# Kernel optimization log

Measured on AMD Instinct MI355X. Metric: run time of the kernel, lower is better.

The kernel has to match this reference:

```python
import jax, jax.numpy as jnp
import numpy as np

PAD = 1          # kernel offsets lie in [-1, 1] for kernel_size=3
COORD_MAX = 128  # coordinates quantized to [0, 128)
S = COORD_MAX + 2 * PAD  # per-dimension encoding stride (130)


def setup_inputs() -> dict:
    key = jax.random.key(0)
    B, N, D = 4, 50000, 3
    coordinates = jax.random.randint(
        jax.random.fold_in(key, 0), (B, N, D), 0, COORD_MAX, dtype=jnp.int32)
    # batch_indices[b, n] == b, matching how the torch code partitions rows
    batch_indices = jnp.broadcast_to(jnp.arange(B, dtype=jnp.int32)[:, None], (B, N))
    # 3^3 hypercube kernel offsets, lexicographic order (KernelGenerator semantics)
    r = jnp.arange(-1, 2, dtype=jnp.int32)
    kernel_offsets = jnp.stack(jnp.meshgrid(r, r, r, indexing='ij'), axis=-1).reshape(-1, 3)
    return {"coordinates": coordinates, "batch_indices": batch_indices,
            "kernel_offsets": kernel_offsets}


def reference(coordinates, batch_indices, kernel_offsets):
    """Vectorized equivalent of LocalSelfAttention.compute_kernel_mapping.

    Returns (input_idx, output_idx, rel_pos_idx, output_key_tensor, num_unique).
    The first three are [B, N, K] (the torch kernel_map flattened row-major is
    exactly zip of these), output_key_tensor is [L, D] padded with -1 beyond
    num_unique rows, with unique keys in first-occurrence (insertion) order --
    identical to the Python dict-hashing loop.
    """
    B, N, D = coordinates.shape
    K = kernel_offsets.shape[0]
    L = B * N * K

    # neighbor coords per (point, offset): [B, N, K, D]
    nb = coordinates[:, :, None, :] + kernel_offsets[None, None, :, :]

    # encode (batch_id, neighbor_coord) into a single int32 key
    enc = jnp.broadcast_to(batch_indices[:, :, None], (B, N, K)).astype(jnp.int32)
    for d in range(D):
        enc = enc * S + (nb[..., d] + PAD)  # max ~ 4*130^3 < 2^31
    keys = enc.reshape(L)

    # sort-based dedup preserving first-occurrence order
    order = jnp.argsort(keys, stable=True)              # [L]
    sk = keys[order]
    new_group = jnp.concatenate([jnp.ones((1,), bool), sk[1:] != sk[:-1]])
    gid_sorted = jnp.cumsum(new_group.astype(jnp.int32)) - 1  # group id per sorted slot
    num_unique = gid_sorted[-1] + 1

    # first flat position where each group's key occurs (empty groups -> int32 max)
    first_occ = jax.ops.segment_min(order, gid_sorted, num_segments=L)
    # insertion-order index of each group (padded groups stably rank last)
    group_rank = jnp.argsort(jnp.argsort(first_occ))

    # scatter group ids back to original flat order, then map to insertion rank
    gid = jnp.zeros((L,), jnp.int32).at[order].set(gid_sorted)
    output_idx = group_rank[gid].reshape(B, N, K).astype(jnp.int32)

    # representative encoded key per group, reordered to insertion order
    rep_key = jax.ops.segment_min(sk, gid_sorted, num_segments=L)
    enc_ord = jnp.zeros((L,), keys.dtype).at[group_rank].set(rep_key)

    # decode neighbor coordinates (drop the batch component, as torch does)
    coords_dec = []
    e = enc_ord
    for _ in range(D):
        coords_dec.append(e % S - PAD)
        e = e // S
    out_coords = jnp.stack(coords_dec[::-1], axis=-1)  # [L, D]
    valid = (jnp.arange(L) < num_unique)[:, None]
    output_key_tensor = jnp.where(valid, out_coords, -1)

    input_idx = jnp.broadcast_to(jnp.arange(N, dtype=jnp.int32)[None, :, None], (B, N, K))
    rel_pos_idx = jnp.broadcast_to(jnp.arange(K, dtype=jnp.int32)[None, None, :], (B, N, K))
    return (input_idx, output_idx, rel_pos_idx, output_key_tensor, num_unique)
```

## Files before the change

kernel.cpp:

```cpp
#include <hip/hip_runtime.h>
#include <cstdint>

#define B_   4
#define N_   50000
#define K_   27
#define P_   (B_ * N_)
#define L_   (P_ * K_)
#define S_   130
#define PL_  (S_ * S_)
#define KS_  (B_ * S_ * S_ * S_)
#define W_   (L_ / 64)
#define NBW  ((W_ + 255) / 256)
#define BIGP 0x7f7f7f7f

__global__ __launch_bounds__(256) void k_init(int4* __restrict__ T4) {
    const int n4 = KS_ / 4;
    int4 v = make_int4(BIGP, BIGP, BIGP, BIGP);
    for (int i = blockIdx.x * blockDim.x + threadIdx.x; i < n4; i += gridDim.x * blockDim.x)
        T4[i] = v;
}

__global__ __launch_bounds__(256) void k_ptab(const int* __restrict__ coords,
                                              const int* __restrict__ bidx,
                                              int* __restrict__ P1,
                                              int* __restrict__ bpt) {
    int p = blockIdx.x * blockDim.x + threadIdx.x;
    if (p >= P_) return;
    int b = bidx[p];
    int x = coords[3 * p + 0] + 1;
    int y = coords[3 * p + 1] + 1;
    int z = coords[3 * p + 2] + 1;
    int idx = ((b * S_ + x) * S_ + y) * S_ + z;
    bpt[p] = idx;
    atomicMin(&P1[idx], p << 5);
}

__global__ __launch_bounds__(512) void k_zy(const int* __restrict__ src,
                                            int* __restrict__ dst) {
    __shared__ int pl[PL_];
    __shared__ int tz[PL_];
    const int4* s4 = (const int4*)(src + (size_t)blockIdx.x * PL_);
    int4* d4       = (int4*)(dst + (size_t)blockIdx.x * PL_);
    int4* pl4      = (int4*)pl;
    for (int i = threadIdx.x; i < PL_ / 4; i += 512) pl4[i] = s4[i];
    __syncthreads();
    for (int i = threadIdx.x; i < PL_; i += 512) {
        int z = i % S_;
        int v = pl[i] + 1;
        if (z > 0)      v = min(v, pl[i - 1] + 2);
        if (z < S_ - 1) v = min(v, pl[i + 1]);
        tz[i] = v;
    }
    __syncthreads();
    for (int i = threadIdx.x; i < PL_ / 4; i += 512) {
        int4 o;
        int base = 4 * i;
        #pragma unroll
        for (int j = 0; j < 4; ++j) {
            int idx = base + j;
            int y = idx / S_;
            int v = tz[idx] + 3;
            if (y > 0)      v = min(v, tz[idx - S_] + 6);
            if (y < S_ - 1) v = min(v, tz[idx + S_]);
            ((int*)&o)[j] = v;
        }
        d4[i] = o;
    }
}

__global__ __launch_bounds__(256) void k_x(const int4* __restrict__ src,
                                           int4* __restrict__ dst) {
    const int n4 = KS_ / 4;
    int i = blockIdx.x * blockDim.x + threadIdx.x;
    if (i >= n4) return;
    int x = (i / (PL_ / 4)) % S_;
    int4 c = src[i];
    int4 v = make_int4(c.x + 9, c.y + 9, c.z + 9, c.w + 9);
    if (x > 0) {
        int4 m = src[i - PL_ / 4];
        v.x = min(v.x, m.x + 18); v.y = min(v.y, m.y + 18);
        v.z = min(v.z, m.z + 18); v.w = min(v.w, m.w + 18);
    }
    if (x < S_ - 1) {
        int4 pp = src[i + PL_ / 4];
        v.x = min(v.x, pp.x); v.y = min(v.y, pp.y);
        v.z = min(v.z, pp.z); v.w = min(v.w, pp.w);
    }
    dst[i] = v;
}

__global__ __launch_bounds__(256) void k_gather(const int* __restrict__ bpt,
                                                const int* __restrict__ M,
                                                int* __restrict__ mArr,
                                                unsigned long long* __restrict__ bitmap,
                                                int* __restrict__ out0,
                                                int* __restrict__ out2) {
    int l = blockIdx.x * blockDim.x + threadIdx.x;
    if (l >= L_) return;
    int p = l / K_;
    int k = l - p * K_;
    out0[l] = p - (p / N_) * N_;
    out2[l] = k;
    int dx = k / 9, dy = (k / 3) % 3, dz = k - (k / 3) * 3;
    int idx = bpt[p] + (dx - 1) * PL_ + (dy - 1) * S_ + (dz - 1);
    int m32 = M[idx];
    mArr[l] = m32;
    unsigned long long bal = __ballot(m32 == ((p << 5) | k));
    if ((threadIdx.x & 63) == 0) bitmap[l >> 6] = bal;
}

__global__ __launch_bounds__(256) void k_scan_words(const unsigned long long* __restrict__ bitmap,
                                                    int* __restrict__ wpre,
                                                    int* __restrict__ bsum) {
    __shared__ int sh[256];
    int w = blockIdx.x * 256 + threadIdx.x;
    int c = (w < W_) ? __popcll(bitmap[w]) : 0;
    sh[threadIdx.x] = c;
    __syncthreads();
    for (int off = 1; off < 256; off <<= 1) {
        int t = (threadIdx.x >= off) ? sh[threadIdx.x - off] : 0;
        __syncthreads();
        sh[threadIdx.x] += t;
        __syncthreads();
    }
    if (w < W_) wpre[w] = sh[threadIdx.x] - c;
    if (threadIdx.x == 255) bsum[blockIdx.x] = sh[255];
}

__global__ __launch_bounds__(512) void k_scan_block(int* __restrict__ bsum,
                                                    int* __restrict__ num_unique_out) {
    __shared__ int sh[512];
    int i = threadIdx.x;
    int v = (i < NBW) ? bsum[i] : 0;
    sh[i] = v;
    __syncthreads();
    for (int off = 1; off < 512; off <<= 1) {
        int t = (i >= off) ? sh[i - off] : 0;
        __syncthreads();
        sh[i] += t;
        __syncthreads();
    }
    if (i < NBW) bsum[i] = sh[i] - v;
    if (i == 0) num_unique_out[0] = sh[511];
}

__global__ __launch_bounds__(256) void k_finalize(const int* __restrict__ coords,
                                                  const int* __restrict__ koffs,
                                                  const unsigned long long* __restrict__ bitmap,
                                                  const int* __restrict__ wpre,
                                                  const int* __restrict__ bsum,
                                                  const int* __restrict__ numuniq,
                                                  int* __restrict__ out1,
                                                  int* __restrict__ outkey) {
    int l = blockIdx.x * blockDim.x + threadIdx.x;
    if (l >= L_) return;
    int m32 = out1[l];
    int m = (m32 >> 5) * K_ + (m32 & 31);
    int w = m >> 6;
    unsigned long long word = bitmap[w];
    unsigned long long mask = (1ull << (m & 63)) - 1ull;
    int rank = wpre[w] + bsum[w >> 8] + (int)__popcll(word & mask);
    out1[l] = rank;
    if (m == l) {
        int p = l / K_;
        int k = l - p * K_;
        outkey[3 * rank + 0] = coords[3 * p + 0] + koffs[3 * k + 0];
        outkey[3 * rank + 1] = coords[3 * p + 1] + koffs[3 * k + 1];
        outkey[3 * rank + 2] = coords[3 * p + 2] + koffs[3 * k + 2];
    }
    if (l >= numuniq[0]) {
        outkey[3 * l + 0] = -1;
        outkey[3 * l + 1] = -1;
        outkey[3 * l + 2] = -1;
    }
}

extern "C" void kernel_launch(void* const* d_in, const int* in_sizes, int n_in,
                              void* d_out, int out_size, void* d_ws, size_t ws_size,
                              hipStream_t stream) {
    const int* coords = (const int*)d_in[0];
    const int* bidx   = (const int*)d_in[1];
    const int* koffs  = (const int*)d_in[2];

    int* out      = (int*)d_out;
    int* out0     = out;
    int* out1     = out + L_;
    int* out2     = out + 2 * L_;
    int* outkey   = out + 3 * L_;
    int* numuniq  = out + 6 * L_;

    int* P1 = (int*)d_ws;
    unsigned long long* bitmap = (unsigned long long*)(P1 + KS_);
    int* wpre = (int*)(bitmap + W_);
    int* bsum = wpre + W_;
    int* bpt  = bsum + NBW;

    int* A = outkey;

    k_init       <<<2048, 256, 0, stream>>>((int4*)P1);
    k_ptab       <<<(P_ + 255) / 256, 256, 0, stream>>>(coords, bidx, P1, bpt);
    k_zy         <<<B_ * S_, 512, 0, stream>>>(P1, A);
    k_x          <<<(KS_ / 4 + 255) / 256, 256, 0, stream>>>((const int4*)A, (int4*)P1);
    k_gather     <<<(L_ + 255) / 256, 256, 0, stream>>>(bpt, P1, out1, bitmap, out0, out2);
    k_scan_words <<<NBW, 256, 0, stream>>>(bitmap, wpre, bsum);
    k_scan_block <<<1, 512, 0, stream>>>(bsum, numuniq);
    k_finalize   <<<(L_ + 255) / 256, 256, 0, stream>>>(coords, koffs, bitmap, wpre, bsum,
                                                        numuniq, out1, outkey);
}
```

Measured before the change: 143.8 us.

## Bucket points by x-plane and build dense table in LDS, dropping global init

Replaces the full-volume global initialization and global atomicMin point table with a counting sort of points into (batch, x) planes. Each z/y pass block then builds its plane's min table in shared memory from its bucket of points. This removes one full write and one full read of the ~35 MB dense table. In exchange it adds four small kernels (zero, histogram, scan, scatter), two of them single-block, which add launch latency. The packed bpt encoding also changes, so the gather kernel recomputes the table index.

```diff
diff --git a/kernel.cpp b/kernel.cpp
--- a/kernel.cpp
+++ b/kernel.cpp
@@ -12,37 +12,68 @@
 #define W_   (L_ / 64)
 #define NBW  ((W_ + 255) / 256)
 #define BIGP 0x7f7f7f7f
-
-__global__ __launch_bounds__(256) void k_init(int4* __restrict__ T4) {
-    const int n4 = KS_ / 4;
-    int4 v = make_int4(BIGP, BIGP, BIGP, BIGP);
-    for (int i = blockIdx.x * blockDim.x + threadIdx.x; i < n4; i += gridDim.x * blockDim.x)
-        T4[i] = v;
-}
-
-__global__ __launch_bounds__(256) void k_ptab(const int* __restrict__ coords,
+#define NBIN (B_ * S_)
+
+__global__ __launch_bounds__(1024) void k_zero(int* __restrict__ hist) {
+    int i = threadIdx.x;
+    if (i < NBIN) hist[i] = 0;
+}
+
+__global__ __launch_bounds__(256) void k_hist(const int* __restrict__ coords,
                                               const int* __restrict__ bidx,
-                                              int* __restrict__ P1,
-                                              int* __restrict__ bpt) {
+                                              int* __restrict__ hist) {
+    int p = blockIdx.x * blockDim.x + threadIdx.x;
+    if (p >= P_) return;
+    atomicAdd(&hist[bidx[p] * S_ + coords[3 * p] + 1], 1);
+}
+
+__global__ __launch_bounds__(1024) void k_hscan(const int* __restrict__ hist,
+                                                int* __restrict__ binoff,
+                                                int* __restrict__ cursor) {
+    __shared__ int sh[1024];
+    int i = threadIdx.x;
+    int v = (i < NBIN) ? hist[i] : 0;
+    sh[i] = v;
+    __syncthreads();
+    for (int off = 1; off < 1024; off <<= 1) {
+        int t = (i >= off) ? sh[i - off] : 0;
+        __syncthreads();
+        sh[i] += t;
+        __syncthreads();
+    }
+    if (i < NBIN) { binoff[i] = sh[i] - v; cursor[i] = sh[i] - v; }
+    if (i == 0) binoff[NBIN] = sh[1023];
+}
+
+__global__ __launch_bounds__(256) void k_scatter(const int* __restrict__ coords,
+                                                 const int* __restrict__ bidx,
+                                                 int* __restrict__ cursor,
+                                                 int2* __restrict__ pts,
+                                                 int* __restrict__ bpt) {
     int p = blockIdx.x * blockDim.x + threadIdx.x;
     if (p >= P_) return;
     int b = bidx[p];
     int x = coords[3 * p + 0] + 1;
     int y = coords[3 * p + 1] + 1;
     int z = coords[3 * p + 2] + 1;
-    int idx = ((b * S_ + x) * S_ + y) * S_ + z;
-    bpt[p] = idx;
-    atomicMin(&P1[idx], p << 5);
-}
-
-__global__ __launch_bounds__(512) void k_zy(const int* __restrict__ src,
+    bpt[p] = (b << 24) | (x << 16) | (y << 8) | z;
+    int slot = atomicAdd(&cursor[b * S_ + x], 1);
+    pts[slot] = make_int2(y * S_ + z, p << 5);
+}
+
+__global__ __launch_bounds__(512) void k_zy(const int2* __restrict__ pts,
+                                            const int* __restrict__ binoff,
                                             int* __restrict__ dst) {
     __shared__ int pl[PL_];
     __shared__ int tz[PL_];
-    const int4* s4 = (const int4*)(src + (size_t)blockIdx.x * PL_);
-    int4* d4       = (int4*)(dst + (size_t)blockIdx.x * PL_);
-    int4* pl4      = (int4*)pl;
-    for (int i = threadIdx.x; i < PL_ / 4; i += 512) pl4[i] = s4[i];
+    int blk = blockIdx.x;
+    for (int i = threadIdx.x; i < PL_; i += 512) pl[i] = BIGP;
+    __syncthreads();
+    int s = binoff[blk], e = binoff[blk + 1];
+    for (int i = s + threadIdx.x; i < e; i += 512) {
+        int2 q = pts[i];
+        atomicMin(&pl[q.x], q.y);
+    }
     __syncthreads();
     for (int i = threadIdx.x; i < PL_; i += 512) {
         int z = i % S_;
@@ -52,6 +83,7 @@
         tz[i] = v;
     }
     __syncthreads();
+    int4* d4 = (int4*)(dst + (size_t)blk * PL_);
     for (int i = threadIdx.x; i < PL_ / 4; i += 512) {
         int4 o;
         int base = 4 * i;
@@ -101,8 +133,11 @@
     int k = l - p * K_;
     out0[l] = p - (p / N_) * N_;
     out2[l] = k;
+    unsigned u = (unsigned)bpt[p];
+    int b = u >> 24, x = (u >> 16) & 255, y = (u >> 8) & 255, z = u & 255;
     int dx = k / 9, dy = (k / 3) % 3, dz = k - (k / 3) * 3;
-    int idx = bpt[p] + (dx - 1) * PL_ + (dy - 1) * S_ + (dz - 1);
+    int cx = x + dx - 1, cy = y + dy - 1, cz = z + dz - 1;
+    int idx = ((b * S_ + cx) * S_ + cy) * S_ + cz;
     int m32 = M[idx];
     mArr[l] = m32;
     unsigned long long bal = __ballot(m32 == ((p << 5) | k));
@@ -189,19 +224,25 @@
     int* outkey   = out + 3 * L_;
     int* numuniq  = out + 6 * L_;
 
-    int* P1 = (int*)d_ws;
-    unsigned long long* bitmap = (unsigned long long*)(P1 + KS_);
-    int* wpre = (int*)(bitmap + W_);
-    int* bsum = wpre + W_;
-    int* bpt  = bsum + NBW;
+    int* M = (int*)d_ws;
+    unsigned long long* bitmap = (unsigned long long*)(M + KS_);
+    int* wpre   = (int*)(bitmap + W_);
+    int* bsum   = wpre + W_;
+    int* bpt    = bsum + NBW;
+    int* hist   = bpt + P_;
+    int* binoff = hist + NBIN;
+    int* cursor = binoff + NBIN + 1;
+    int2* pts   = (int2*)(cursor + NBIN + 1);
 
     int* A = outkey;
 
-    k_init       <<<2048, 256, 0, stream>>>((int4*)P1);
-    k_ptab       <<<(P_ + 255) / 256, 256, 0, stream>>>(coords, bidx, P1, bpt);
-    k_zy         <<<B_ * S_, 512, 0, stream>>>(P1, A);
-    k_x          <<<(KS_ / 4 + 255) / 256, 256, 0, stream>>>((const int4*)A, (int4*)P1);
-    k_gather     <<<(L_ + 255) / 256, 256, 0, stream>>>(bpt, P1, out1, bitmap, out0, out2);
+    k_zero       <<<1, 1024, 0, stream>>>(hist);
+    k_hist       <<<(P_ + 255) / 256, 256, 0, stream>>>(coords, bidx, hist);
+    k_hscan      <<<1, 1024, 0, stream>>>(hist, binoff, cursor);
+    k_scatter    <<<(P_ + 255) / 256, 256, 0, stream>>>(coords, bidx, cursor, pts, bpt);
+    k_zy         <<<NBIN, 512, 0, stream>>>(pts, binoff, A);
+    k_x          <<<(KS_ / 4 + 255) / 256, 256, 0, stream>>>((const int4*)A, (int4*)M);
+    k_gather     <<<(L_ + 255) / 256, 256, 0, stream>>>(bpt, M, out1, bitmap, out0, out2);
     k_scan_words <<<NBW, 256, 0, stream>>>(bitmap, wpre, bsum);
     k_scan_block <<<1, 512, 0, stream>>>(bsum, numuniq);
     k_finalize   <<<(L_ + 255) / 256, 256, 0, stream>>>(coords, koffs, bitmap, wpre, bsum,
```

Result: slower. 226.4 us (+57.5%).
